# Performance work log

Hardware: AMD Instinct MI355X
Metric: run time of the kernel (lower is better)

Reference implementation:

```python
import jax, jax.numpy as jnp
import numpy as np

N_NODES = 50000
N_EDGES = 1600000
IN_DIM = 128
HEADS = 8
OUT_C = 16  # per-head channels; HEADS*OUT_C == IN_DIM -> residual active
NEG_SLOPE = 0.2
BN_EPS = 1e-5


def setup_inputs() -> dict:
    key = jax.random.key(0)
    ks = jax.random.split(key, 8)
    x = jax.random.normal(ks[0], (N_NODES, IN_DIM), dtype=jnp.float32)
    edge_index = jax.random.randint(ks[1], (2, N_EDGES), 0, N_NODES, dtype=jnp.int64)
    # GATConv params (PyG: shared lin for src/dst on single-tensor input)
    W = jax.random.normal(ks[2], (IN_DIM, HEADS * OUT_C), dtype=jnp.float32) / np.sqrt(IN_DIM)
    att_src = jax.random.normal(ks[3], (HEADS, OUT_C), dtype=jnp.float32) / np.sqrt(OUT_C)
    att_dst = jax.random.normal(ks[4], (HEADS, OUT_C), dtype=jnp.float32) / np.sqrt(OUT_C)
    bias = jnp.zeros((HEADS * OUT_C,), dtype=jnp.float32)
    # BatchNorm1d affine params
    gamma = jnp.ones((HEADS * OUT_C,), dtype=jnp.float32)
    beta = jnp.zeros((HEADS * OUT_C,), dtype=jnp.float32)
    return {"x": x, "edge_index": edge_index, "W": W, "att_src": att_src,
            "att_dst": att_dst, "bias": bias, "gamma": gamma, "beta": beta}


def reference(x, edge_index, W, att_src, att_dst, bias, gamma, beta):
    N = x.shape[0]
    H, C = att_src.shape
    src, dst = edge_index[0], edge_index[1]

    xl = (x @ W).reshape(N, H, C)                      # [N,H,C]
    a_src = jnp.sum(xl * att_src[None], axis=-1)       # [N,H]
    a_dst = jnp.sum(xl * att_dst[None], axis=-1)       # [N,H]

    e = jax.nn.leaky_relu(a_src[src] + a_dst[dst], NEG_SLOPE)  # [E,H]
    # segment softmax over incoming edges of each dst node
    m = jax.ops.segment_max(e, dst, num_segments=N)    # [N,H], -inf for empty
    m = jnp.where(jnp.isfinite(m), m, 0.0)
    ex = jnp.exp(e - m[dst])                           # [E,H]
    denom = jax.ops.segment_sum(ex, dst, num_segments=N)
    alpha = ex / (denom[dst] + 1e-16)                  # [E,H]

    out = jax.ops.segment_sum(alpha[:, :, None] * xl[src], dst, num_segments=N)  # [N,H,C]
    h = out.reshape(N, H * C) + bias

    # BatchNorm1d (training mode: batch statistics, biased variance)
    mean = jnp.mean(h, axis=0)
    var = jnp.mean((h - mean) ** 2, axis=0)
    h = (h - mean) * jax.lax.rsqrt(var + BN_EPS) * gamma + beta

    h = jax.nn.relu(h)
    return x + h  # residual (in_dim == H*C)
```

## Files before the change

kernel.cpp:

```cpp
#include <hip/hip_runtime.h>
#include <hip/hip_fp16.h>
#include <math.h>

#define N_NODES 50000
#define N_EDGES 1600000
#define DIM 128
#define HEADS 8
#define NEG_SLOPE 0.2f
#define BN_EPS 1e-5f

typedef _Float16 f16x8 __attribute__((ext_vector_type(8)));
typedef float f32x4 __attribute__((ext_vector_type(4)));

#define NBUCK 196
#define SEGCAP 12288
#define CHUNK 8192
#define NB_A ((N_EDGES + CHUNK - 1) / CHUNK)
#define LIN_NB ((N_NODES + 127) / 128)
#define FUSED_NB (NB_A + LIN_NB)

struct BinAShm {
    int hist[NBUCK], excl[NBUCK], gbase[NBUCK], cnt2[NBUCK];
    int sc[256];
    unsigned int buf[CHUNK];
};
struct LinShm { __half wh[16384]; };

__global__ __launch_bounds__(512) void k_linbinA(
        const float* __restrict__ x, const float* __restrict__ W,
        const float* __restrict__ att_s, const float* __restrict__ att_d,
        const int* __restrict__ ei, int* __restrict__ bcur,
        unsigned int* __restrict__ pairs, __half* __restrict__ xlh,
        float* __restrict__ a_src, float* __restrict__ a_dst) {
    __shared__ union { BinAShm a; LinShm l; } sh;
    const int t = threadIdx.x;

    if (blockIdx.x < NB_A) {
        const int base = blockIdx.x * CHUNK;
        const int cnt = min(CHUNK, N_EDGES - base);

        for (int j = t; j < NBUCK; j += 512) { sh.a.hist[j] = 0; sh.a.cnt2[j] = 0; }
        __syncthreads();
        for (int i = t * 4; i < cnt; i += 2048) {
            const int4 dv = *(const int4*)(ei + N_EDGES + base + i);
            atomicAdd(&sh.a.hist[dv.x >> 8], 1);
            atomicAdd(&sh.a.hist[dv.y >> 8], 1);
            atomicAdd(&sh.a.hist[dv.z >> 8], 1);
            atomicAdd(&sh.a.hist[dv.w >> 8], 1);
        }
        __syncthreads();
        if (t < 256) sh.a.sc[t] = (t < NBUCK) ? sh.a.hist[t] : 0;
        __syncthreads();
        for (int d = 1; d < 256; d <<= 1) {
            int xo = 0;
            if (t < 256 && t >= d) xo = sh.a.sc[t - d];
            __syncthreads();
            if (t < 256) sh.a.sc[t] += xo;
            __syncthreads();
        }
        if (t < NBUCK) {
            sh.a.excl[t] = sh.a.sc[t] - sh.a.hist[t];
            sh.a.gbase[t] = t * SEGCAP + atomicAdd(&bcur[t], sh.a.hist[t]);
        }
        __syncthreads();
        for (int i = t * 4; i < cnt; i += 2048) {
            const int4 sv = *(const int4*)(ei + base + i);
            const int4 dv = *(const int4*)(ei + N_EDGES + base + i);
            const int ss[4] = {sv.x, sv.y, sv.z, sv.w};
            const int dd[4] = {dv.x, dv.y, dv.z, dv.w};
            #pragma unroll
            for (int k = 0; k < 4; ++k) {
                const int b = dd[k] >> 8;
                const int r = atomicAdd(&sh.a.cnt2[b], 1);
                sh.a.buf[sh.a.excl[b] + r] = (unsigned int)ss[k]
                    | ((unsigned int)(dd[k] & 255) << 16) | ((unsigned int)b << 24);
            }
        }
        __syncthreads();
        for (int i = t; i < cnt; i += 512) {
            const unsigned int u = sh.a.buf[i];
            const int b = u >> 24;
            pairs[sh.a.gbase[b] + (i - sh.a.excl[b])] = u & 0xFFFFFF;
        }
    } else {
        for (int v = t; v < 2048; v += 512) {
            const int g = v >> 6, lane = v & 63;
            const int nt = g >> 2, kt = g & 3;
            const int q = lane >> 4, n = lane & 15;
            #pragma unroll
            for (int j = 0; j < 8; ++j)
                sh.l.wh[(size_t)(g * 64 + lane) * 8 + j] =
                    __float2half(W[(kt * 32 + q * 8 + j) * DIM + nt * 16 + n]);
        }
        __syncthreads();

        const int wave = t >> 6;
        const int lane = t & 63;
        const int q = lane >> 4, n = lane & 15;
        const int nb = ((blockIdx.x - NB_A) * 8 + wave) * 16;

        const int rowA = min(nb + n, N_NODES - 1);
        const float* xr = x + (size_t)rowA * DIM;
        f16x8 a[4];
        #pragma unroll
        for (int kt = 0; kt < 4; ++kt) {
            const float4 p0 = *(const float4*)(xr + kt * 32 + q * 8);
            const float4 p1 = *(const float4*)(xr + kt * 32 + q * 8 + 4);
            a[kt][0] = (_Float16)p0.x; a[kt][1] = (_Float16)p0.y;
            a[kt][2] = (_Float16)p0.z; a[kt][3] = (_Float16)p0.w;
            a[kt][4] = (_Float16)p1.x; a[kt][5] = (_Float16)p1.y;
            a[kt][6] = (_Float16)p1.z; a[kt][7] = (_Float16)p1.w;
        }

        f32x4 acc[8];
        #pragma unroll
        for (int nt = 0; nt < 8; ++nt) acc[nt] = (f32x4){0.f, 0.f, 0.f, 0.f};

        const f16x8* wb = (const f16x8*)sh.l.wh;
        #pragma unroll
        for (int nt = 0; nt < 8; ++nt) {
            #pragma unroll
            for (int kt = 0; kt < 4; ++kt) {
                const f16x8 b = wb[(nt * 4 + kt) * 64 + lane];
                acc[nt] = __builtin_amdgcn_mfma_f32_16x16x32_f16(a[kt], b, acc[nt], 0, 0, 0);
            }
        }

        const int r0 = nb + q * 4;
        #pragma unroll
        for (int nt = 0; nt < 8; ++nt) {
            const float as = att_s[nt * 16 + n];
            const float ad = att_d[nt * 16 + n];
            #pragma unroll
            for (int r = 0; r < 4; ++r) {
                const int row = r0 + r;
                const float v = acc[nt][r];
                float s = v * as;
                float d = v * ad;
                #pragma unroll
                for (int off = 8; off; off >>= 1) {
                    s += __shfl_xor(s, off, 16);
                    d += __shfl_xor(d, off, 16);
                }
                if (row < N_NODES) {
                    xlh[(size_t)row * DIM + nt * 16 + n] = __float2half(v);
                    if (n == 0) {
                        a_src[row * HEADS + nt] = s * 1.44269504f;
                        a_dst[row * HEADS + nt] = d * 1.44269504f;
                    }
                }
            }
        }
    }
}

__global__ __launch_bounds__(1024) void k_binB(const unsigned int* __restrict__ pairs,
                                               const int* __restrict__ bcur,
                                               unsigned short* __restrict__ csr,
                                               int2* __restrict__ nrange,
                                               float* __restrict__ gsums) {
    __shared__ int hist[256], eh[256], excl[256], cnt2[256];
    __shared__ int plen;
    __shared__ unsigned short out[SEGCAP];
    const int t = threadIdx.x;
    const int b = blockIdx.x;
    if (b == 0 && t < 256) gsums[t] = 0.f;
    const int lo = b * SEGCAP;
    const int cnt = bcur[b];

    if (t < 256) { hist[t] = 0; cnt2[t] = 0; }
    __syncthreads();
    for (int i = t; i < cnt; i += 1024)
        atomicAdd(&hist[pairs[lo + i] >> 16], 1);
    __syncthreads();
    if (t < 256) { eh[t] = (hist[t] + 1) & ~1; excl[t] = eh[t]; }
    __syncthreads();
    for (int d = 1; d < 256; d <<= 1) {
        int xo = 0;
        if (t < 256 && t >= d) xo = excl[t - d];
        __syncthreads();
        if (t < 256) excl[t] += xo;
        __syncthreads();
    }
    if (t < 256) excl[t] -= eh[t];
    if (t == 255) plen = excl[255] + eh[255];
    __syncthreads();
    for (int i = t; i < cnt; i += 1024) {
        const unsigned int u = pairs[lo + i];
        const int dl = u >> 16;
        const int r = atomicAdd(&cnt2[dl], 1);
        out[excl[dl] + r] = (unsigned short)(u & 0xFFFF);
    }
    __syncthreads();
    const int pl = plen;
    for (int i = t; i < pl; i += 1024)
        csr[2 * lo + i] = out[i];
    if (t < 256) {
        const int node = (b << 8) + t;
        if (node < N_NODES) {
            int2 rg;
            rg.x = 2 * lo + excl[t];
            rg.y = rg.x + hist[t];
            nrange[node] = rg;
        }
    }
}

#define AGG_NB (N_NODES / 4)

__global__ void k_aggr7(const int2* __restrict__ nrange,
                        const unsigned short* __restrict__ csr,
                        const float* __restrict__ a_src, const float* __restrict__ a_dst,
                        const __half* __restrict__ xlh, float* __restrict__ y) {
    const int d = blockIdx.x * 4 + (threadIdx.x >> 6);
    const int lane = threadIdx.x & 63;
    const int g = lane >> 4;
    const int cl = lane & 15;
    const int h = cl >> 1;
    const int2 rg = nrange[d];
    const int lo = rg.x, hi = rg.y;
    const float ad = a_dst[d * HEADS + h];

    float acc[8];
    #pragma unroll
    for (int k = 0; k < 8; ++k) acc[k] = 0.f;
    float dsum = 0.f;

    int i = lo;
    for (; i + 8 <= hi; i += 8) {
        const int s0 = csr[i + g];
        const int s1 = csr[i + 4 + g];
        const float as0 = a_src[s0 * HEADS + h];
        const float as1 = a_src[s1 * HEADS + h];
        const f16x8 x0 = *(const f16x8*)(xlh + (size_t)s0 * DIM + cl * 8);
        const f16x8 x1 = *(const f16x8*)(xlh + (size_t)s1 * DIM + cl * 8);
        const float e0 = as0 + ad;
        const float e1 = as1 + ad;
        const float w0 = exp2f(fmaxf(e0, NEG_SLOPE * e0));
        const float w1 = exp2f(fmaxf(e1, NEG_SLOPE * e1));
        dsum += w0 + w1;
        #pragma unroll
        for (int k = 0; k < 8; ++k) acc[k] = fmaf(w0, (float)x0[k], acc[k]);
        #pragma unroll
        for (int k = 0; k < 8; ++k) acc[k] = fmaf(w1, (float)x1[k], acc[k]);
    }
    for (; i < hi; i += 4) {
        const int idx = i + g;
        const int sv = csr[min(idx, hi - 1)];
        const float e = a_src[sv * HEADS + h] + ad;
        const f16x8 xv = *(const f16x8*)(xlh + (size_t)sv * DIM + cl * 8);
        float w = exp2f(fmaxf(e, NEG_SLOPE * e));
        if (idx >= hi) w = 0.f;
        dsum += w;
        #pragma unroll
        for (int k = 0; k < 8; ++k) acc[k] = fmaf(w, (float)xv[k], acc[k]);
    }
    #pragma unroll
    for (int k = 0; k < 8; ++k) {
        acc[k] += __shfl_xor(acc[k], 16);
        acc[k] += __shfl_xor(acc[k], 32);
    }
    dsum += __shfl_xor(dsum, 16);
    dsum += __shfl_xor(dsum, 32);
    const float inv = 1.f / (dsum + 1e-16f);
    float2 o;
    o.x = acc[2 * g] * inv;
    o.y = acc[2 * g + 1] * inv;
    *(float2*)(y + (size_t)d * DIM + cl * 8 + g * 2) = o;
}

__global__ void k_stats(const float* __restrict__ y, const float* __restrict__ bias,
                        float* __restrict__ gsums) {
    const int c = threadIdx.x;
    const float b = bias[c];
    float s = 0.f, ss = 0.f;
    for (int n = blockIdx.x; n < N_NODES; n += gridDim.x) {
        const float h = y[n * DIM + c] + b;
        s += h;
        ss += h * h;
    }
    atomicAdd(&gsums[c], s);
    atomicAdd(&gsums[DIM + c], ss);
}

__global__ void k_final(float* __restrict__ y, const float* __restrict__ x,
                        const float* __restrict__ sums, const float* __restrict__ sumsq,
                        const float* __restrict__ gamma, const float* __restrict__ beta,
                        const float* __restrict__ bias) {
    const int q = blockIdx.x * blockDim.x + threadIdx.x;
    const int cq = q & (DIM / 4 - 1);
    const float4 sm = ((const float4*)sums)[cq];
    const float4 sq = ((const float4*)sumsq)[cq];
    const float4 gm = ((const float4*)gamma)[cq];
    const float4 bt = ((const float4*)beta)[cq];
    const float4 bs = ((const float4*)bias)[cq];
    float4 v = ((const float4*)y)[q];
    const float4 xv = ((const float4*)x)[q];
    const float inv_n = 1.f / (float)N_NODES;
#define BNC(c) { const float mean = sm.c * inv_n;                         \
                 const float var = sq.c * inv_n - mean * mean;            \
                 const float sc = rsqrtf(var + BN_EPS) * gm.c;            \
                 const float sh = bt.c + (bs.c - mean) * sc;              \
                 v.c = xv.c + fmaxf(v.c * sc + sh, 0.f); }
    BNC(x) BNC(y) BNC(z) BNC(w)
#undef BNC
    ((float4*)y)[q] = v;
}

extern "C" void kernel_launch(void* const* d_in, const int* in_sizes, int n_in,
                              void* d_out, int out_size, void* d_ws, size_t ws_size,
                              hipStream_t stream) {
    const float* x     = (const float*)d_in[0];
    const int*   ei    = (const int*)  d_in[1];
    const float* W     = (const float*)d_in[2];
    const float* att_s = (const float*)d_in[3];
    const float* att_d = (const float*)d_in[4];
    const float* bias  = (const float*)d_in[5];
    const float* gamma = (const float*)d_in[6];
    const float* beta  = (const float*)d_in[7];
    float* y = (float*)d_out;

    __half* xlh  = (__half*)d_ws;
    float* a_src = (float*)(xlh + (size_t)N_NODES * DIM);
    float* a_dst = a_src + (size_t)N_NODES * HEADS;
    float* sums  = a_dst + (size_t)N_NODES * HEADS;
    float* sumsq = sums  + DIM;
    int*   bcur  = (int*)(sumsq + DIM);
    int2*  nrange = (int2*)(bcur + 256);
    unsigned int* pairs = (unsigned int*)(nrange + N_NODES);
    unsigned short* csr = (unsigned short*)pairs;

    hipMemsetAsync(bcur, 0, 256 * sizeof(int), stream);
    k_linbinA<<<FUSED_NB, 512, 0, stream>>>(x, W, att_s, att_d, ei, bcur, pairs,
                                            xlh, a_src, a_dst);
    k_binB<<<NBUCK, 1024, 0, stream>>>(pairs, bcur, csr, nrange, sums);
    k_aggr7<<<AGG_NB, 256, 0, stream>>>(nrange, csr, a_src, a_dst, xlh, y);
    k_stats<<<512, DIM, 0, stream>>>(y, bias, sums);
    k_final<<<(size_t)N_NODES * DIM / 4 / 256, 256, 0, stream>>>(y, x, sums, sumsq,
                                                                 gamma, beta, bias);
}
```

Before: 230.7 us.

## Split xl into four head-pair planes and aggregate each plane in separate passes

The linear kernel now writes the fp16 projected features as four 32-channel planes, each holding two heads, instead of one row-major 128-channel array. The aggregation kernel launches four passes over the nodes, one per plane. In each pass a wavefront covers 16 edges at a time with 4 lanes per edge. The aim is a smaller gather working set per pass, so plane-sized feature tables stay in cache (L2/MALL) during random-access gathers. The cost is reading the CSR ranges, indices and attention scores four times, plus extra shuffle reductions and lower lane utilization on nodes with few edges.

```diff
diff --git a/kernel.cpp b/kernel.cpp
--- a/kernel.cpp
+++ b/kernel.cpp
@@ -131,6 +131,8 @@
         for (int nt = 0; nt < 8; ++nt) {
             const float as = att_s[nt * 16 + n];
             const float ad = att_d[nt * 16 + n];
+            const int qq = nt >> 1;
+            const int wi = (nt & 1) * 16 + n;
             #pragma unroll
             for (int r = 0; r < 4; ++r) {
                 const int row = r0 + r;
@@ -143,7 +145,8 @@
                     d += __shfl_xor(d, off, 16);
                 }
                 if (row < N_NODES) {
-                    xlh[(size_t)row * DIM + nt * 16 + n] = __float2half(v);
+                    xlh[(size_t)qq * (N_NODES * 32) + (size_t)row * 32 + wi] =
+                        __float2half(v);
                     if (n == 0) {
                         a_src[row * HEADS + nt] = s * 1.44269504f;
                         a_dst[row * HEADS + nt] = d * 1.44269504f;
@@ -207,16 +210,20 @@
 }
 
 #define AGG_NB (N_NODES / 4)
-
-__global__ void k_aggr7(const int2* __restrict__ nrange,
+#define AGG_TOTAL_NB (4 * AGG_NB)
+
+__global__ void k_aggr8(const int2* __restrict__ nrange,
                         const unsigned short* __restrict__ csr,
                         const float* __restrict__ a_src, const float* __restrict__ a_dst,
                         const __half* __restrict__ xlh, float* __restrict__ y) {
-    const int d = blockIdx.x * 4 + (threadIdx.x >> 6);
+    const int pass = blockIdx.x / AGG_NB;
+    const int nb   = blockIdx.x - pass * AGG_NB;
+    const int d = nb * 4 + (threadIdx.x >> 6);
     const int lane = threadIdx.x & 63;
-    const int g = lane >> 4;
-    const int cl = lane & 15;
-    const int h = cl >> 1;
+    const int g = lane >> 2;
+    const int cl = lane & 3;
+    const int h = 2 * pass + (cl >> 1);
+    const __half* xq = xlh + (size_t)pass * (N_NODES * 32);
     const int2 rg = nrange[d];
     const int lo = rg.x, hi = rg.y;
     const float ad = a_dst[d * HEADS + h];
@@ -227,13 +234,13 @@
     float dsum = 0.f;
 
     int i = lo;
-    for (; i + 8 <= hi; i += 8) {
+    for (; i + 32 <= hi; i += 32) {
         const int s0 = csr[i + g];
-        const int s1 = csr[i + 4 + g];
+        const int s1 = csr[i + 16 + g];
         const float as0 = a_src[s0 * HEADS + h];
         const float as1 = a_src[s1 * HEADS + h];
-        const f16x8 x0 = *(const f16x8*)(xlh + (size_t)s0 * DIM + cl * 8);
-        const f16x8 x1 = *(const f16x8*)(xlh + (size_t)s1 * DIM + cl * 8);
+        const f16x8 x0 = *(const f16x8*)(xq + (size_t)s0 * 32 + cl * 8);
+        const f16x8 x1 = *(const f16x8*)(xq + (size_t)s1 * 32 + cl * 8);
         const float e0 = as0 + ad;
         const float e1 = as1 + ad;
         const float w0 = exp2f(fmaxf(e0, NEG_SLOPE * e0));
@@ -244,11 +251,21 @@
         #pragma unroll
         for (int k = 0; k < 8; ++k) acc[k] = fmaf(w1, (float)x1[k], acc[k]);
     }
-    for (; i < hi; i += 4) {
+    for (; i + 16 <= hi; i += 16) {
+        const int s0 = csr[i + g];
+        const float as0 = a_src[s0 * HEADS + h];
+        const f16x8 x0 = *(const f16x8*)(xq + (size_t)s0 * 32 + cl * 8);
+        const float e0 = as0 + ad;
+        const float w0 = exp2f(fmaxf(e0, NEG_SLOPE * e0));
+        dsum += w0;
+        #pragma unroll
+        for (int k = 0; k < 8; ++k) acc[k] = fmaf(w0, (float)x0[k], acc[k]);
+    }
+    if (i < hi) {
         const int idx = i + g;
-        const int sv = csr[min(idx, hi - 1)];
+        const int sv = csr[idx < hi ? idx : hi - 1];
         const float e = a_src[sv * HEADS + h] + ad;
-        const f16x8 xv = *(const f16x8*)(xlh + (size_t)sv * DIM + cl * 8);
+        const f16x8 xv = *(const f16x8*)(xq + (size_t)sv * 32 + cl * 8);
         float w = exp2f(fmaxf(e, NEG_SLOPE * e));
         if (idx >= hi) w = 0.f;
         dsum += w;
@@ -257,16 +274,23 @@
     }
     #pragma unroll
     for (int k = 0; k < 8; ++k) {
+        acc[k] += __shfl_xor(acc[k], 4);
+        acc[k] += __shfl_xor(acc[k], 8);
         acc[k] += __shfl_xor(acc[k], 16);
         acc[k] += __shfl_xor(acc[k], 32);
     }
+    dsum += __shfl_xor(dsum, 4);
+    dsum += __shfl_xor(dsum, 8);
     dsum += __shfl_xor(dsum, 16);
     dsum += __shfl_xor(dsum, 32);
     const float inv = 1.f / (dsum + 1e-16f);
-    float2 o;
-    o.x = acc[2 * g] * inv;
-    o.y = acc[2 * g + 1] * inv;
-    *(float2*)(y + (size_t)d * DIM + cl * 8 + g * 2) = o;
+    if (lane < 16) {
+        const int j = g & 3;
+        float2 o;
+        o.x = acc[2 * j] * inv;
+        o.y = acc[2 * j + 1] * inv;
+        *(float2*)(y + (size_t)d * DIM + pass * 32 + cl * 8 + 2 * j) = o;
+    }
 }
 
 __global__ void k_stats(const float* __restrict__ y, const float* __restrict__ bias,
@@ -334,7 +358,7 @@
     k_linbinA<<<FUSED_NB, 512, 0, stream>>>(x, W, att_s, att_d, ei, bcur, pairs,
                                             xlh, a_src, a_dst);
     k_binB<<<NBUCK, 1024, 0, stream>>>(pairs, bcur, csr, nrange, sums);
-    k_aggr7<<<AGG_NB, 256, 0, stream>>>(nrange, csr, a_src, a_dst, xlh, y);
+    k_aggr8<<<AGG_TOTAL_NB, 256, 0, stream>>>(nrange, csr, a_src, a_dst, xlh, y);
     k_stats<<<512, DIM, 0, stream>>>(y, bias, sums);
     k_final<<<(size_t)N_NODES * DIM / 4 / 256, 256, 0, stream>>>(y, x, sums, sumsq,
                                                                  gamma, beta, bias);
```

Result: slower. 261.2 us (+13.3%).
